# Kernel tuning notes

Hardware: AMD Instinct MI355X
Metric: run time of the kernel (lower is better)

The kernel has to match this reference:

```python
import jax, jax.numpy as jnp
import numpy as np

N, C, H, W = 8, 64, 128, 128
CO, K = 64, 3
BN_EPS = 1e-5
POW_EPS = 1e-12  # keeps |x|**alpha differentiable at 0


def setup_inputs() -> dict:
    key = jax.random.key(0)
    k1, k2, k3, k4 = jax.random.split(key, 4)
    x = jax.random.normal(k1, (N, C, H, W), jnp.float32)
    weight = jax.random.normal(k2, (CO, C, K, K), jnp.float32) * 0.1
    gamma = 1.0 + 0.1 * jax.random.normal(k3, (C,), jnp.float32)
    beta = 0.1 * jax.random.normal(k4, (C,), jnp.float32)
    alpha = jnp.float32(1.0)  # learnable power of PowerActivation (AdderSR)
    return {"x": x, "weight": weight, "gamma": gamma, "beta": beta, "alpha": alpha}


def adder2d(x, weight):
    """AdderNet conv: out[n,co,h,w] = -sum_{ci,kh,kw} |patch - W[co,ci,kh,kw]|."""
    co, ci, kh, kw = weight.shape
    # [N, C*kh*kw, H, W], channel-major feature layout matches weight.reshape(co, -1)
    patches = jax.lax.conv_general_dilated_patches(
        x, (kh, kw), (1, 1), padding=((1, 1), (1, 1)))
    wflat = weight.reshape(co, -1)

    def per_out_channel(w):  # w: [C*kh*kw]
        return -jnp.sum(jnp.abs(patches - w[None, :, None, None]), axis=1)  # [N,H,W]

    out = jax.lax.map(per_out_channel, wflat)  # [CO, N, H, W] (sequential -> bounded memory)
    return jnp.transpose(out, (1, 0, 2, 3))    # [N, CO, H, W]


def reference(x, weight, gamma, beta, alpha):
    y = adder2d(x, weight) + x  # residual add
    # BatchNorm2d in training mode: batch statistics over (N, H, W)
    mean = jnp.mean(y, axis=(0, 2, 3), keepdims=True)
    var = jnp.var(y, axis=(0, 2, 3), keepdims=True)
    y = (y - mean) * jax.lax.rsqrt(var + BN_EPS)
    y = y * gamma[None, :, None, None] + beta[None, :, None, None]
    # PowerActivation: sign(x) * |x|^alpha (learnable alpha)
    return jnp.sign(y) * jnp.power(jnp.abs(y) + POW_EPS, alpha)
```

## Files before the change

kernel.cpp:

```cpp
#include <hip/hip_runtime.h>
#include <math.h>

#define N_   8
#define C_   64
#define H_   128
#define W_   128
#define HW_  (H_ * W_)
#define CHW_ (C_ * HW_)
#define K_   3
#define CI_TILE 4
#define CO_BLK  8
#define N_CG    (C_ / CO_BLK)
#define TILE_H 16
#define TILE_W 32
#define HALO_H (TILE_H + 2)
#define HALO_W (TILE_W + 2)
#define XSTR   36
#define CISZ   (HALO_H * XSTR)
#define PLANE  (HALO_H * HALO_W)
#define NSLOT  5
#define WROW 12
#define WCI  (CO_BLK * WROW)
#define WSTRIDE (C_ * K_ * K_)
#define BN_EPS 1e-5
#define POW_EPS 1e-12f

#define MAC_TERM(accv, wv, xvk) do { float t_;                         \
    asm("v_sub_f32 %1, %2, %3\n\t"                                     \
        "v_add_f32 %0, %0, |%1|"                                       \
        : "+v"(accv), "=&v"(t_)                                        \
        : "v"(wv), "v"(xvk));                                          \
  } while (0)

__global__ __launch_bounds__(128, 4) void adder_kernel(
    const float* __restrict__ x, const float* __restrict__ weight,
    float* __restrict__ y, double* __restrict__ sums)
{
    __shared__ __align__(16) float sx[CI_TILE * CISZ];
    __shared__ __align__(16) float wl[CI_TILE * WCI];
    __shared__ float red[CO_BLK][2][2];

    const int tx = threadIdx.x & 15;
    const int ty = threadIdx.x >> 4;
    const int tile_h = blockIdx.x >> 2;
    const int tile_w = blockIdx.x & 3;
    const int n   = blockIdx.y;
    const int co0 = blockIdx.z * CO_BLK;
    const int h0 = tile_h * TILE_H;
    const int w0 = tile_w * TILE_W;

    float a00[CO_BLK], a01[CO_BLK], a10[CO_BLK], a11[CO_BLK];
#pragma unroll
    for (int j = 0; j < CO_BLK; ++j) { a00[j]=0.f; a01[j]=0.f; a10[j]=0.f; a11[j]=0.f; }

    const float* xn = x + n * CHW_;

    int lx[NSLOT], gx[NSLOT];
#pragma unroll
    for (int s = 0; s < NSLOT; ++s) {
        int idx = threadIdx.x + s * 128;
        if (idx < PLANE) {
            int r = idx / HALO_W, c = idx - r * HALO_W;
            int gh = h0 + r - 1, gw = w0 + c - 1;
            lx[s] = r * XSTR + c;
            gx[s] = ((unsigned)gh < (unsigned)H_ && (unsigned)gw < (unsigned)W_)
                    ? (gh * W_ + gw) : -1;
        } else { lx[s] = -1; gx[s] = -1; }
    }
    int wlo = -1, wgo = 0;
    if (threadIdx.x < CO_BLK * 9) {
        int co = threadIdx.x / 9, k = threadIdx.x - co * 9;
        wlo = co * WROW + k;
        wgo = (co0 + co) * WSTRIDE + k;
    }

    for (int cb = 0; cb < C_; cb += CI_TILE) {
        const float* xncb = xn + cb * HW_;
        __syncthreads();
#pragma unroll
        for (int ci = 0; ci < CI_TILE; ++ci) {
#pragma unroll
            for (int s = 0; s < NSLOT; ++s) {
                if (lx[s] >= 0) {
                    float v = (gx[s] >= 0) ? xncb[ci * HW_ + gx[s]] : 0.f;
                    sx[ci * CISZ + lx[s]] = v;
                }
            }
        }
        if (wlo >= 0) {
            const float* wgp = weight + wgo + cb * 9;
#pragma unroll
            for (int ci = 0; ci < CI_TILE; ++ci)
                wl[ci * WCI + wlo] = wgp[ci * 9];
        }
        __syncthreads();

#pragma unroll 1
        for (int ci = 0; ci < CI_TILE; ++ci) {
            const float* sxc = &sx[ci * CISZ];
            float xv[4][4];
#pragma unroll
            for (int r = 0; r < 4; ++r) {
                float2 a = *(const float2*)(sxc + (2 * ty + r) * XSTR + 2 * tx);
                float2 b = *(const float2*)(sxc + (2 * ty + r) * XSTR + 2 * tx + 2);
                xv[r][0] = a.x; xv[r][1] = a.y; xv[r][2] = b.x; xv[r][3] = b.y;
            }

            const float* wrow = &wl[ci * WCI];
#pragma unroll
            for (int j = 0; j < CO_BLK; ++j) {
                float4 wa = *(const float4*)(wrow + j * WROW);
                float4 wb = *(const float4*)(wrow + j * WROW + 4);
                float  w8 = wrow[j * WROW + 8];
                MAC_TERM(a00[j], wa.x, xv[0][0]); MAC_TERM(a01[j], wa.x, xv[0][1]);
                MAC_TERM(a10[j], wa.x, xv[1][0]); MAC_TERM(a11[j], wa.x, xv[1][1]);
                MAC_TERM(a00[j], wa.y, xv[0][1]); MAC_TERM(a01[j], wa.y, xv[0][2]);
                MAC_TERM(a10[j], wa.y, xv[1][1]); MAC_TERM(a11[j], wa.y, xv[1][2]);
                MAC_TERM(a00[j], wa.z, xv[0][2]); MAC_TERM(a01[j], wa.z, xv[0][3]);
                MAC_TERM(a10[j], wa.z, xv[1][2]); MAC_TERM(a11[j], wa.z, xv[1][3]);
                MAC_TERM(a00[j], wa.w, xv[1][0]); MAC_TERM(a01[j], wa.w, xv[1][1]);
                MAC_TERM(a10[j], wa.w, xv[2][0]); MAC_TERM(a11[j], wa.w, xv[2][1]);
                MAC_TERM(a00[j], wb.x, xv[1][1]); MAC_TERM(a01[j], wb.x, xv[1][2]);
                MAC_TERM(a10[j], wb.x, xv[2][1]); MAC_TERM(a11[j], wb.x, xv[2][2]);
                MAC_TERM(a00[j], wb.y, xv[1][2]); MAC_TERM(a01[j], wb.y, xv[1][3]);
                MAC_TERM(a10[j], wb.y, xv[2][2]); MAC_TERM(a11[j], wb.y, xv[2][3]);
                MAC_TERM(a00[j], wb.z, xv[2][0]); MAC_TERM(a01[j], wb.z, xv[2][1]);
                MAC_TERM(a10[j], wb.z, xv[3][0]); MAC_TERM(a11[j], wb.z, xv[3][1]);
                MAC_TERM(a00[j], wb.w, xv[2][1]); MAC_TERM(a01[j], wb.w, xv[2][2]);
                MAC_TERM(a10[j], wb.w, xv[3][1]); MAC_TERM(a11[j], wb.w, xv[3][2]);
                MAC_TERM(a00[j], w8,   xv[2][2]); MAC_TERM(a01[j], w8,   xv[2][3]);
                MAC_TERM(a10[j], w8,   xv[3][2]); MAC_TERM(a11[j], w8,   xv[3][3]);
            }
        }
    }

    const int r0 = h0 + 2 * ty, c0 = w0 + 2 * tx;
    float* yo = y + n * CHW_ + co0 * HW_ + r0 * W_ + c0;
    const float* xrp = xn + co0 * HW_ + r0 * W_ + c0;
    const int lane = threadIdx.x & 63;
    const int wid  = threadIdx.x >> 6;

#pragma unroll
    for (int j = 0; j < CO_BLK; ++j) {
        float2 rv0 = *(const float2*)(xrp + j * HW_);
        float2 rv1 = *(const float2*)(xrp + j * HW_ + W_);
        float v00 = -a00[j] + rv0.x, v01 = -a01[j] + rv0.y;
        float v10 = -a10[j] + rv1.x, v11 = -a11[j] + rv1.y;
        float2 o0; o0.x = v00; o0.y = v01;
        float2 o1; o1.x = v10; o1.y = v11;
        *(float2*)(yo + j * HW_)      = o0;
        *(float2*)(yo + j * HW_ + W_) = o1;
        float s  = v00 + v01 + v10 + v11;
        float ss = v00 * v00 + v01 * v01 + v10 * v10 + v11 * v11;
#pragma unroll
        for (int off = 32; off > 0; off >>= 1) {
            s  += __shfl_down(s, off);
            ss += __shfl_down(ss, off);
        }
        if (lane == 0) { red[j][0][wid] = s; red[j][1][wid] = ss; }
    }
    __syncthreads();
    if (threadIdx.x < CO_BLK) {
        int j = threadIdx.x;
        float S  = red[j][0][0] + red[j][0][1];
        float SS = red[j][1][0] + red[j][1][1];
        atomicAdd(&sums[co0 + j], (double)S);
        atomicAdd(&sums[C_ + co0 + j], (double)SS);
    }
}

__global__ void finalize_kernel(const double* __restrict__ sums,
                                const float* __restrict__ gamma,
                                const float* __restrict__ beta,
                                float* __restrict__ sc)
{
    const int c = threadIdx.x;
    const double cnt = (double)(N_ * HW_);
    double mean = sums[c] / cnt;
    double var  = sums[C_ + c] / cnt - mean * mean;
    float inv   = (float)(1.0 / sqrt(var + (double)BN_EPS));
    float scale = gamma[c] * inv;
    float shift = beta[c] - (float)mean * scale;
    sc[c]      = scale;
    sc[C_ + c] = shift;
}

__global__ __launch_bounds__(256) void apply_kernel(
    float* __restrict__ y, const float* __restrict__ sc,
    const float* __restrict__ alpha_p)
{
    const int idx = blockIdx.x * 256 + threadIdx.x;
    const float alpha = alpha_p[0];
    const int e0 = idx * 4;
    const int c = (e0 / HW_) & (C_ - 1);
    const float scale = sc[c];
    const float shift = sc[C_ + c];

    float4 v = reinterpret_cast<float4*>(y)[idx];
    float* pv = reinterpret_cast<float*>(&v);
    if (alpha == 1.0f) {
#pragma unroll
        for (int i = 0; i < 4; ++i)
            pv[i] = pv[i] * scale + shift;
    } else {
#pragma unroll
        for (int i = 0; i < 4; ++i) {
            float t = pv[i] * scale + shift;
            float sgn = (t > 0.f) ? 1.f : ((t < 0.f) ? -1.f : 0.f);
            pv[i] = sgn * powf(fabsf(t) + POW_EPS, alpha);
        }
    }
    reinterpret_cast<float4*>(y)[idx] = v;
}

extern "C" void kernel_launch(void* const* d_in, const int* in_sizes, int n_in,
                              void* d_out, int out_size, void* d_ws, size_t ws_size,
                              hipStream_t stream)
{
    const float* x      = (const float*)d_in[0];
    const float* weight = (const float*)d_in[1];
    const float* gamma  = (const float*)d_in[2];
    const float* beta   = (const float*)d_in[3];
    const float* alpha  = (const float*)d_in[4];
    float* out = (float*)d_out;

    double* sums = (double*)d_ws;
    float*  sc   = (float*)((char*)d_ws + 128 * sizeof(double));

    hipMemsetAsync(d_ws, 0, 128 * sizeof(double), stream);

    adder_kernel<<<dim3(32, N_, N_CG), 128, 0, stream>>>(x, weight, out, sums);
    finalize_kernel<<<1, C_, 0, stream>>>(sums, gamma, beta, sc);

    const int n4 = (N_ * CHW_) / 4;
    apply_kernel<<<n4 / 256, 256, 0, stream>>>(out, sc, alpha);
}
```

Baseline: 301.4 us.

## Load input patches directly from global memory instead of staging in LDS

Removes the shared-memory halo tile for the input and has each thread read its 4x4 neighbourhood straight from global memory using precomputed clamped offsets and zero masks. Weights are now staged in larger 32-channel chunks, so a block synchronises twice instead of sixteen times. The goal is to cut LDS traffic and barrier overhead. The cost is 16 uncoalesced-ish global/cache loads per channel per thread with heavy overlap between neighbours, which relies on L1/L2 to absorb the redundancy, plus extra registers for offsets and masks.

```diff
diff --git a/kernel.cpp b/kernel.cpp
--- a/kernel.cpp
+++ b/kernel.cpp
@@ -8,19 +8,12 @@
 #define HW_  (H_ * W_)
 #define CHW_ (C_ * HW_)
 #define K_   3
-#define CI_TILE 4
 #define CO_BLK  8
 #define N_CG    (C_ / CO_BLK)
 #define TILE_H 16
 #define TILE_W 32
-#define HALO_H (TILE_H + 2)
-#define HALO_W (TILE_W + 2)
-#define XSTR   36
-#define CISZ   (HALO_H * XSTR)
-#define PLANE  (HALO_H * HALO_W)
-#define NSLOT  5
 #define WROW 12
-#define WCI  (CO_BLK * WROW)
+#define WCHUNK 32
 #define WSTRIDE (C_ * K_ * K_)
 #define BN_EPS 1e-5
 #define POW_EPS 1e-12f
@@ -36,8 +29,7 @@
     const float* __restrict__ x, const float* __restrict__ weight,
     float* __restrict__ y, double* __restrict__ sums)
 {
-    __shared__ __align__(16) float sx[CI_TILE * CISZ];
-    __shared__ __align__(16) float wl[CI_TILE * WCI];
+    __shared__ __align__(16) float wl[WCHUNK * CO_BLK * WROW];
     __shared__ float red[CO_BLK][2][2];
 
     const int tx = threadIdx.x & 15;
@@ -55,82 +47,69 @@
 
     const float* xn = x + n * CHW_;
 
-    int lx[NSLOT], gx[NSLOT];
-#pragma unroll
-    for (int s = 0; s < NSLOT; ++s) {
-        int idx = threadIdx.x + s * 128;
-        if (idx < PLANE) {
-            int r = idx / HALO_W, c = idx - r * HALO_W;
-            int gh = h0 + r - 1, gw = w0 + c - 1;
-            lx[s] = r * XSTR + c;
-            gx[s] = ((unsigned)gh < (unsigned)H_ && (unsigned)gw < (unsigned)W_)
-                    ? (gh * W_ + gw) : -1;
-        } else { lx[s] = -1; gx[s] = -1; }
-    }
-    int wlo = -1, wgo = 0;
-    if (threadIdx.x < CO_BLK * 9) {
-        int co = threadIdx.x / 9, k = threadIdx.x - co * 9;
-        wlo = co * WROW + k;
-        wgo = (co0 + co) * WSTRIDE + k;
-    }
-
-    for (int cb = 0; cb < C_; cb += CI_TILE) {
-        const float* xncb = xn + cb * HW_;
+    int   off16[16];
+    float msk16[16];
+#pragma unroll
+    for (int r = 0; r < 4; ++r) {
+#pragma unroll
+        for (int c = 0; c < 4; ++c) {
+            int gh = h0 + 2 * ty - 1 + r;
+            int gw = w0 + 2 * tx - 1 + c;
+            bool ok = ((unsigned)gh < (unsigned)H_) && ((unsigned)gw < (unsigned)W_);
+            int ch = gh < 0 ? 0 : (gh > H_ - 1 ? H_ - 1 : gh);
+            int cw = gw < 0 ? 0 : (gw > W_ - 1 ? W_ - 1 : gw);
+            off16[r * 4 + c] = ch * W_ + cw;
+            msk16[r * 4 + c] = ok ? 1.f : 0.f;
+        }
+    }
+
+    for (int half = 0; half < 2; ++half) {
+        const int cb0 = half * WCHUNK;
         __syncthreads();
-#pragma unroll
-        for (int ci = 0; ci < CI_TILE; ++ci) {
-#pragma unroll
-            for (int s = 0; s < NSLOT; ++s) {
-                if (lx[s] >= 0) {
-                    float v = (gx[s] >= 0) ? xncb[ci * HW_ + gx[s]] : 0.f;
-                    sx[ci * CISZ + lx[s]] = v;
-                }
-            }
-        }
-        if (wlo >= 0) {
-            const float* wgp = weight + wgo + cb * 9;
-#pragma unroll
-            for (int ci = 0; ci < CI_TILE; ++ci)
-                wl[ci * WCI + wlo] = wgp[ci * 9];
+        for (int idx = threadIdx.x; idx < WCHUNK * CO_BLK * 9; idx += 128) {
+            int ci = idx / (CO_BLK * 9);
+            int r  = idx - ci * (CO_BLK * 9);
+            int co = r / 9;
+            int k  = r - co * 9;
+            wl[(ci * CO_BLK + co) * WROW + k] =
+                weight[(co0 + co) * WSTRIDE + (cb0 + ci) * 9 + k];
         }
         __syncthreads();
 
+        const float* xp = xn + cb0 * HW_;
 #pragma unroll 1
-        for (int ci = 0; ci < CI_TILE; ++ci) {
-            const float* sxc = &sx[ci * CISZ];
-            float xv[4][4];
-#pragma unroll
-            for (int r = 0; r < 4; ++r) {
-                float2 a = *(const float2*)(sxc + (2 * ty + r) * XSTR + 2 * tx);
-                float2 b = *(const float2*)(sxc + (2 * ty + r) * XSTR + 2 * tx + 2);
-                xv[r][0] = a.x; xv[r][1] = a.y; xv[r][2] = b.x; xv[r][3] = b.y;
-            }
-
-            const float* wrow = &wl[ci * WCI];
+        for (int ci = 0; ci < WCHUNK; ++ci) {
+            float xv[16];
+#pragma unroll
+            for (int i = 0; i < 16; ++i)
+                xv[i] = xp[off16[i]] * msk16[i];
+
+            const float* wrow = &wl[ci * CO_BLK * WROW];
 #pragma unroll
             for (int j = 0; j < CO_BLK; ++j) {
                 float4 wa = *(const float4*)(wrow + j * WROW);
                 float4 wb = *(const float4*)(wrow + j * WROW + 4);
                 float  w8 = wrow[j * WROW + 8];
-                MAC_TERM(a00[j], wa.x, xv[0][0]); MAC_TERM(a01[j], wa.x, xv[0][1]);
-                MAC_TERM(a10[j], wa.x, xv[1][0]); MAC_TERM(a11[j], wa.x, xv[1][1]);
-                MAC_TERM(a00[j], wa.y, xv[0][1]); MAC_TERM(a01[j], wa.y, xv[0][2]);
-                MAC_TERM(a10[j], wa.y, xv[1][1]); MAC_TERM(a11[j], wa.y, xv[1][2]);
-                MAC_TERM(a00[j], wa.z, xv[0][2]); MAC_TERM(a01[j], wa.z, xv[0][3]);
-                MAC_TERM(a10[j], wa.z, xv[1][2]); MAC_TERM(a11[j], wa.z, xv[1][3]);
-                MAC_TERM(a00[j], wa.w, xv[1][0]); MAC_TERM(a01[j], wa.w, xv[1][1]);
-                MAC_TERM(a10[j], wa.w, xv[2][0]); MAC_TERM(a11[j], wa.w, xv[2][1]);
-                MAC_TERM(a00[j], wb.x, xv[1][1]); MAC_TERM(a01[j], wb.x, xv[1][2]);
-                MAC_TERM(a10[j], wb.x, xv[2][1]); MAC_TERM(a11[j], wb.x, xv[2][2]);
-                MAC_TERM(a00[j], wb.y, xv[1][2]); MAC_TERM(a01[j], wb.y, xv[1][3]);
-                MAC_TERM(a10[j], wb.y, xv[2][2]); MAC_TERM(a11[j], wb.y, xv[2][3]);
-                MAC_TERM(a00[j], wb.z, xv[2][0]); MAC_TERM(a01[j], wb.z, xv[2][1]);
-                MAC_TERM(a10[j], wb.z, xv[3][0]); MAC_TERM(a11[j], wb.z, xv[3][1]);
-                MAC_TERM(a00[j], wb.w, xv[2][1]); MAC_TERM(a01[j], wb.w, xv[2][2]);
-                MAC_TERM(a10[j], wb.w, xv[3][1]); MAC_TERM(a11[j], wb.w, xv[3][2]);
-                MAC_TERM(a00[j], w8,   xv[2][2]); MAC_TERM(a01[j], w8,   xv[2][3]);
-                MAC_TERM(a10[j], w8,   xv[3][2]); MAC_TERM(a11[j], w8,   xv[3][3]);
+                MAC_TERM(a00[j], wa.x, xv[0]);  MAC_TERM(a01[j], wa.x, xv[1]);
+                MAC_TERM(a10[j], wa.x, xv[4]);  MAC_TERM(a11[j], wa.x, xv[5]);
+                MAC_TERM(a00[j], wa.y, xv[1]);  MAC_TERM(a01[j], wa.y, xv[2]);
+                MAC_TERM(a10[j], wa.y, xv[5]);  MAC_TERM(a11[j], wa.y, xv[6]);
+                MAC_TERM(a00[j], wa.z, xv[2]);  MAC_TERM(a01[j], wa.z, xv[3]);
+                MAC_TERM(a10[j], wa.z, xv[6]);  MAC_TERM(a11[j], wa.z, xv[7]);
+                MAC_TERM(a00[j], wa.w, xv[4]);  MAC_TERM(a01[j], wa.w, xv[5]);
+                MAC_TERM(a10[j], wa.w, xv[8]);  MAC_TERM(a11[j], wa.w, xv[9]);
+                MAC_TERM(a00[j], wb.x, xv[5]);  MAC_TERM(a01[j], wb.x, xv[6]);
+                MAC_TERM(a10[j], wb.x, xv[9]);  MAC_TERM(a11[j], wb.x, xv[10]);
+                MAC_TERM(a00[j], wb.y, xv[6]);  MAC_TERM(a01[j], wb.y, xv[7]);
+                MAC_TERM(a10[j], wb.y, xv[10]); MAC_TERM(a11[j], wb.y, xv[11]);
+                MAC_TERM(a00[j], wb.z, xv[8]);  MAC_TERM(a01[j], wb.z, xv[9]);
+                MAC_TERM(a10[j], wb.z, xv[12]); MAC_TERM(a11[j], wb.z, xv[13]);
+                MAC_TERM(a00[j], wb.w, xv[9]);  MAC_TERM(a01[j], wb.w, xv[10]);
+                MAC_TERM(a10[j], wb.w, xv[13]); MAC_TERM(a11[j], wb.w, xv[14]);
+                MAC_TERM(a00[j], w8,   xv[10]); MAC_TERM(a01[j], w8,   xv[11]);
+                MAC_TERM(a10[j], w8,   xv[14]); MAC_TERM(a11[j], w8,   xv[15]);
             }
+            xp += HW_;
         }
     }
 
```

After: 315.5 us. 1.05x slower.
